# Kernel optimization log

Hardware: AMD Instinct MI355X
Metric: run time of the kernel (lower is better)

## Reference

```python
import jax, jax.numpy as jnp
import numpy as np

D = 1024
B = 16
SP = 256
T = B * SP
DT_REF = 1.0
MAX_GROWTH = 0.3


def _cayley(re, im):
    A = re + 1j * im
    A = A - A.conj().T  # skew-Hermitian part
    I = jnp.eye(A.shape[0], dtype=A.dtype)
    return jnp.linalg.solve(I + A, I - A)


def _dft_basis(d):
    n = jnp.arange(d)
    k = jnp.arange(d)[:, None]
    ang = -2.0 * jnp.pi * (k * n).astype(jnp.float32) / d
    return jnp.exp(1j * ang) / jnp.sqrt(jnp.float32(d))


def _forward(x_input, h_prev_re, h_prev_im, xg_re, xg_im, flux_re, flux_im, dt,
             u_raw_re, u_raw_im, v_raw_re, v_raw_im, log_sigma, dft_weight,
             decay_re, decay_im, Wi, bi, Wo, bo, Wg, bg,
             ld, lf, law_re, law_im, base_noise, Wu1, bu1, Wu2, bu2,
             noise_re, noise_im):
    d = x_input.shape[-1]
    # ---- basis.encode ----
    V = _cayley(v_raw_re, v_raw_im)                       # [D,D] complex
    s_diag = jnp.exp(log_sigma).astype(V.dtype)
    xc = x_input.astype(jnp.complex64)
    alpha = jax.nn.sigmoid(dft_weight)
    x_tilde = (xc @ V) * s_diag * (1.0 - alpha) + (xc @ _dft_basis(d)) * alpha
    x_tilde = x_tilde[:, None, :]                          # [T,1,D]
    # ---- flux_tracker.forward_step ----
    fdecay = jax.nn.sigmoid(decay_re) + 1j * decay_im
    x_cat = jnp.concatenate([xg_re, xg_im], axis=-1)       # [B,2D]
    xin = x_cat @ Wi.T + bi
    update = xin[..., :d] + 1j * xin[..., d:]
    flux_next = (flux_re + 1j * flux_im) * fdecay + update
    s_cat = jnp.concatenate([flux_next.real, flux_next.imag], axis=-1)
    proj = s_cat @ Wo.T + bo
    source = proj[..., :d] + 1j * proj[..., d:]            # [B,D] complex
    gate = jax.nn.sigmoid(s_cat @ Wg.T + bg)               # [B,D] real
    # ---- transition operators ----
    l_re = jnp.tanh(-jnp.exp(ld) + law_re) * MAX_GROWTH
    lam = l_re + 1j * (lf + law_im)
    dt_ratio = dt / DT_REF                                 # [1]
    op_decay = jnp.exp(lam[None, :] * dt_ratio[:, None].astype(jnp.complex64))
    op_forcing = (op_decay - 1.0) / (lam[None, :] + 1e-8)
    # ---- expand source/gate over spatial ----
    bsz = source.shape[0]
    sp = x_tilde.shape[0] // bsz
    src = jnp.broadcast_to(source[:, None, None, :], (bsz, sp, 1, d)).reshape(-1, 1, d)
    g = jnp.broadcast_to(gate[:, None, None, :], (bsz, sp, 1, d)).reshape(-1, 1, d)
    forcing = x_tilde * g + src * (1.0 - g)
    h_prev = h_prev_re + 1j * h_prev_im
    h_next = h_prev * op_decay + forcing * op_forcing      # [T,1,D]
    # ---- SDE stochastic term ----
    base_var = base_noise ** 2 * jnp.expm1(2.0 * l_re * dt_ratio[:, None]) / (2.0 * l_re + 1e-8)
    base_var = jnp.maximum(base_var, 0.0)                  # [1,D]
    h_mean = h_next.mean(axis=1).real                      # [T,D]
    u = jax.nn.softplus(jax.nn.silu(h_mean @ Wu1.T + bu1) @ Wu2.T + bu2)  # [T,D]
    std = jnp.sqrt(base_var * u)[:, None, :].astype(h_next.dtype)          # [T,1,D]
    noise = (noise_re + 1j * noise_im) * jnp.sqrt(jnp.float32(0.5))
    return h_next + noise * std, flux_next


def setup_inputs() -> dict:
    key = jax.random.key(0)
    ks = jax.random.split(key, 40)
    rn = lambda i, shp, sc=1.0: jax.random.normal(ks[i], shp, jnp.float32) * sc
    q_re = jnp.linalg.qr(rn(0, (D, D)))[0]
    q_im = jnp.linalg.qr(rn(1, (D, D)))[0]
    return {
        "x_input": rn(2, (T, D)),
        "h_prev_re": rn(3, (T, 1, D)), "h_prev_im": rn(4, (T, 1, D)),
        "xg_re": rn(5, (B, D)), "xg_im": rn(6, (B, D)),
        "flux_re": rn(7, (B, D)), "flux_im": rn(8, (B, D)),
        "dt": jnp.ones((1,), jnp.float32),
        "u_raw_re": q_re * 0.1, "u_raw_im": q_im * 0.1,
        "v_raw_re": q_re.T * 0.1, "v_raw_im": q_im.T * 0.1,
        "log_sigma": jnp.zeros((D,), jnp.float32),
        "dft_weight": jnp.float32(0.2),
        "decay_re": rn(9, (D,), 0.1) - 1.0, "decay_im": rn(10, (D,), 0.1),
        "Wi": rn(11, (2 * D, 2 * D), 0.02), "bi": jnp.zeros((2 * D,), jnp.float32),
        "Wo": rn(12, (2 * D, 2 * D), 0.02), "bo": jnp.zeros((2 * D,), jnp.float32),
        "Wg": rn(13, (D, 2 * D), 0.02), "bg": jnp.zeros((D,), jnp.float32),
        "ld": rn(14, (D,), 0.5) - 2.0, "lf": rn(15, (D,), 1.0),
        "law_re": rn(16, (D,), 0.01), "law_im": rn(17, (D,), 0.01),
        "base_noise": jnp.float32(0.01),
        "Wu1": rn(18, (D // 4, D), 0.03), "bu1": jnp.zeros((D // 4,), jnp.float32),
        "Wu2": rn(19, (D, D // 4), 0.06), "bu2": jnp.zeros((D,), jnp.float32),
        "noise_re": rn(20, (T, 1, D)), "noise_im": rn(21, (T, 1, D)),
    }


def reference(x_input, h_prev_re, h_prev_im, xg_re, xg_im, flux_re, flux_im, dt,
              u_raw_re, u_raw_im, v_raw_re, v_raw_im, log_sigma, dft_weight,
              decay_re, decay_im, Wi, bi, Wo, bo, Wg, bg,
              ld, lf, law_re, law_im, base_noise, Wu1, bu1, Wu2, bu2,
              noise_re, noise_im):
    return _forward(x_input, h_prev_re, h_prev_im, xg_re, xg_im, flux_re, flux_im, dt,
                    u_raw_re, u_raw_im, v_raw_re, v_raw_im, log_sigma, dft_weight,
                    decay_re, decay_im, Wi, bi, Wo, bo, Wg, bg,
                    ld, lf, law_re, law_im, base_noise, Wu1, bu1, Wu2, bu2,
                    noise_re, noise_im)
```

## Files before the change

kernel.cpp:

```cpp
#include <hip/hip_runtime.h>
#include <cstddef>

#define TPB 256

typedef short bf8v  __attribute__((ext_vector_type(8)));
typedef float f32x4 __attribute__((ext_vector_type(4)));
typedef unsigned short u16;

#define PSZ 2048
#define PSZ2 4096
#define LSTR 40
#define BUF1 2560
#define CSTR 68
#define RTBUF 12288

static __device__ __forceinline__ u16 f2bf(float x) {
  unsigned int u = __float_as_uint(x);
  u = (u + 0x7FFFu + ((u >> 16) & 1u)) >> 16;
  return (u16)u;
}
static __device__ __forceinline__ float bf2f(u16 x) {
  return __uint_as_float(((unsigned int)x) << 16);
}
static __device__ __forceinline__ float sigmoidf_(float x) {
  return 1.0f / (1.0f + __expf(-x));
}
static __device__ __forceinline__ float spf_(float v) {
  return (v > 15.0f) ? v : __logf(1.0f + __expf(v));
}
static __device__ __forceinline__ bf8v neg8(bf8v a) {
  #pragma unroll
  for (int i = 0; i < 8; ++i) a[i] ^= (short)0x8000;
  return a;
}
static __device__ __forceinline__ void pack8(const float4& x, const float4& y,
                                             u16* dst) {
  unsigned int* d = (unsigned int*)dst;
  d[0] = ((unsigned)f2bf(x.y) << 16) | f2bf(x.x);
  d[1] = ((unsigned)f2bf(x.w) << 16) | f2bf(x.z);
  d[2] = ((unsigned)f2bf(y.y) << 16) | f2bf(y.x);
  d[3] = ((unsigned)f2bf(y.w) << 16) | f2bf(y.z);
}
static __device__ __forceinline__ uint2 packbf4(float a, float b, float c, float d) {
  uint2 r;
  r.x = ((unsigned)f2bf(b) << 16) | f2bf(a);
  r.y = ((unsigned)f2bf(d) << 16) | f2bf(c);
  return r;
}
static __device__ __forceinline__ void gload16(const u16* g, u16* l) {
  __builtin_amdgcn_global_load_lds((const __attribute__((address_space(1))) void*)g,
                                   (__attribute__((address_space(3))) void*)l,
                                   16, 0, 0);
}
static __device__ __forceinline__ bf8v fragld(const u16* plane, int r, int kq) {
  int kb = (kq << 4) ^ (((r >> 1) & 3) << 4);
  return *(const bf8v*)(plane + r * 32 + (kb >> 1));
}
static __device__ __forceinline__ bf8v fragld2(const u16* plane, int r, int kq, int s) {
  int ch = ((s << 2) + kq) ^ (r & 7);
  return *(const bf8v*)(plane + r * 64 + (ch << 3));
}
static __device__ __forceinline__ int swz8(int flat, int T) {
  return (flat & 7) * (T >> 3) + (flat >> 3);
}

#define WAITV(n) asm volatile("s_waitcnt vmcnt(" #n ")" ::: "memory")

__global__ __launch_bounds__(TPB) void build_a_k(
    const float* __restrict__ vre, const float* __restrict__ vim,
    u16* __restrict__ Ar, u16* __restrict__ Ai,
    u16* __restrict__ Nr, u16* __restrict__ Ni)
{
  int idx = blockIdx.x * TPB + threadIdx.x;
  int i = idx >> 10, j = idx & 1023;
  float ar = vre[idx] - vre[j * 1024 + i];
  float ai = vim[idx] + vim[j * 1024 + i];
  float dg = (i == j) ? 1.0f : 0.0f;
  Ar[idx] = f2bf(ar);       Ai[idx] = f2bf(ai);
  Nr[idx] = f2bf(dg - ar);  Ni[idx] = f2bf(-ai);
}

#define CG_VARS                                                              \
  int lane = tid & 63;                                                       \
  int wr = (tid >> 7) & 1, wc = (tid >> 6) & 1;                              \
  int lr8_ = ((tid & 63) >> 3) + ((tid >> 6) << 4);                          \
  int ks2_ = (((lane & 7) ^ (lane >> 3)) << 3);                              \
  u16* Lw_ = lds + ((tid >> 6) << 10);                                       \
  f32x4 accR[2][2] = {};                                                     \
  f32x4 accI[2][2] = {};

#define CG_STAGE(buf, k0, PAr, PAi, PBr, PBi)                                \
  { u16* Lb = Lw_ + (buf) * (4 * PSZ2);                                      \
    gload16((PAr) + (size_t)(bm + lr8_) * 1024 + (k0) + ks2_,     Lb + 0 * PSZ2);       \
    gload16((PAr) + (size_t)(bm + lr8_ + 8) * 1024 + (k0) + ks2_, Lb + 0 * PSZ2 + 512); \
    gload16((PAi) + (size_t)(bm + lr8_) * 1024 + (k0) + ks2_,     Lb + 1 * PSZ2);       \
    gload16((PAi) + (size_t)(bm + lr8_ + 8) * 1024 + (k0) + ks2_, Lb + 1 * PSZ2 + 512); \
    gload16((PBr) + (size_t)(bn + lr8_) * 1024 + (k0) + ks2_,     Lb + 2 * PSZ2);       \
    gload16((PBr) + (size_t)(bn + lr8_ + 8) * 1024 + (k0) + ks2_, Lb + 2 * PSZ2 + 512); \
    gload16((PBi) + (size_t)(bn + lr8_) * 1024 + (k0) + ks2_,     Lb + 3 * PSZ2);       \
    gload16((PBi) + (size_t)(bn + lr8_ + 8) * 1024 + (k0) + ks2_, Lb + 3 * PSZ2 + 512); }

#define CG_FRAGS(buf, s)                                                     \
  const u16* L = lds + (buf) * (4 * PSZ2);                                   \
  int rA = wr * 32 + (lane & 15);                                            \
  int rB = wc * 32 + (lane & 15);                                            \
  int kq = lane >> 4;                                                        \
  bf8v ar[2], ai[2], br[2], bi[2];                                           \
  ar[0] = fragld2(L + 0 * PSZ2, rA, kq, s);  ar[1] = fragld2(L + 0 * PSZ2, rA + 16, kq, s); \
  ai[0] = fragld2(L + 1 * PSZ2, rA, kq, s);  ai[1] = fragld2(L + 1 * PSZ2, rA + 16, kq, s); \
  br[0] = fragld2(L + 2 * PSZ2, rB, kq, s);  br[1] = fragld2(L + 2 * PSZ2, rB + 16, kq, s); \
  bi[0] = fragld2(L + 3 * PSZ2, rB, kq, s);  bi[1] = fragld2(L + 3 * PSZ2, rB + 16, kq, s);

#define CG_MFMA_BNEG1                                                        \
  { bf8v nbi[2] = { neg8(bi[0]), neg8(bi[1]) };                              \
    _Pragma("unroll")                                                        \
    for (int mf = 0; mf < 2; ++mf)                                           \
      _Pragma("unroll")                                                      \
      for (int nf = 0; nf < 2; ++nf) {                                       \
        accR[mf][nf] = __builtin_amdgcn_mfma_f32_16x16x32_bf16(ar[mf], br[nf],  accR[mf][nf], 0, 0, 0); \
        accR[mf][nf] = __builtin_amdgcn_mfma_f32_16x16x32_bf16(ai[mf], bi[nf],  accR[mf][nf], 0, 0, 0); \
        accI[mf][nf] = __builtin_amdgcn_mfma_f32_16x16x32_bf16(ar[mf], nbi[nf], accI[mf][nf], 0, 0, 0); \
        accI[mf][nf] = __builtin_amdgcn_mfma_f32_16x16x32_bf16(ai[mf], br[nf],  accI[mf][nf], 0, 0, 0); \
      } }

#define CG_PIPELINE(MFMA_OP, PAr, PAi, PBr, PBi)                             \
  CG_STAGE(0, 0, PAr, PAi, PBr, PBi);                                        \
  _Pragma("unroll 1")                                                        \
  for (int t = 0; t < 16; ++t) {                                             \
    int bufc = t & 1;                                                        \
    if (t + 1 < 16) { CG_STAGE(bufc ^ 1, (t + 1) * 64, PAr, PAi, PBr, PBi);  \
                      WAITV(8); }                                            \
    else            { WAITV(0); }                                            \
    __builtin_amdgcn_sched_barrier(0);                                       \
    __builtin_amdgcn_s_barrier();                                            \
    __builtin_amdgcn_s_setprio(1);                                           \
    { CG_FRAGS(bufc, 0) MFMA_OP }                                            \
    { CG_FRAGS(bufc, 1) MFMA_OP }                                            \
    __builtin_amdgcn_s_setprio(0);                                           \
    __builtin_amdgcn_sched_barrier(0);                                       \
    __builtin_amdgcn_s_barrier();                                            \
  }

#define CGRT_VARS                                                            \
  int lane = tid & 63;                                                       \
  int wv = tid >> 6;                                                         \
  int wr = wv >> 1, wc = wv & 1;                                             \
  int ln8 = lane >> 3;                                                       \
  int ks2_ = (((lane & 7) ^ ln8) << 3);                                      \
  f32x4 accR[2] = {};                                                        \
  f32x4 accI[2] = {};

#define CGRT_STAGE(buf, k0, PAr, PAi, PBr, PBi)                              \
  { u16* Lb = lds + (buf) * RTBUF;                                           \
    _Pragma("unroll")                                                        \
    for (int j = 0; j < 6; ++j) {                                            \
      int idx = wv * 6 + j;                                                  \
      const u16* src; int row; int doff;                                     \
      if (idx < 16) {                                                        \
        int pl = idx >> 3, gr = idx & 7;                                     \
        src = pl ? (PAi) : (PAr);                                            \
        row = bm + gr * 8 + ln8;                                             \
        doff = pl * 4096 + gr * 512;                                         \
      } else {                                                               \
        int i2 = idx - 16;                                                   \
        int pl = i2 >> 2, gr = i2 & 3;                                       \
        src = pl ? (PBi) : (PBr);                                            \
        row = bn + gr * 8 + ln8;                                             \
        doff = 8192 + pl * 2048 + gr * 512;                                  \
      }                                                                      \
      gload16(src + (size_t)row * 1024 + (k0) + ks2_, Lb + doff);            \
    } }

#define CGRT_FRAGS(buf, s)                                                   \
  const u16* L = lds + (buf) * RTBUF;                                        \
  int rA = wr * 32 + (lane & 15);                                            \
  int rB = wc * 16 + (lane & 15);                                            \
  int kq = lane >> 4;                                                        \
  bf8v ar[2], ai[2], br1, bi1;                                               \
  ar[0] = fragld2(L, rA, kq, s);          ar[1] = fragld2(L, rA + 16, kq, s);          \
  ai[0] = fragld2(L + 4096, rA, kq, s);   ai[1] = fragld2(L + 4096, rA + 16, kq, s);   \
  br1 = fragld2(L + 8192, rB, kq, s);                                        \
  bi1 = fragld2(L + 10240, rB, kq, s);

#define CGRT_MFMA_BNEG0                                                      \
  { bf8v nbr = neg8(br1);                                                    \
    bf8v nbi = neg8(bi1);                                                    \
    _Pragma("unroll")                                                        \
    for (int mf = 0; mf < 2; ++mf) {                                         \
      accR[mf] = __builtin_amdgcn_mfma_f32_16x16x32_bf16(ar[mf], nbr, accR[mf], 0, 0, 0); \
      accR[mf] = __builtin_amdgcn_mfma_f32_16x16x32_bf16(ai[mf], nbi, accR[mf], 0, 0, 0); \
      accI[mf] = __builtin_amdgcn_mfma_f32_16x16x32_bf16(ar[mf], bi1, accI[mf], 0, 0, 0); \
      accI[mf] = __builtin_amdgcn_mfma_f32_16x16x32_bf16(ai[mf], nbr, accI[mf], 0, 0, 0); \
    } }

#define CGRT_MFMA_BNEG1                                                      \
  { bf8v nbi = neg8(bi1);                                                    \
    _Pragma("unroll")                                                        \
    for (int mf = 0; mf < 2; ++mf) {                                         \
      accR[mf] = __builtin_amdgcn_mfma_f32_16x16x32_bf16(ar[mf], br1, accR[mf], 0, 0, 0); \
      accR[mf] = __builtin_amdgcn_mfma_f32_16x16x32_bf16(ai[mf], bi1, accR[mf], 0, 0, 0); \
      accI[mf] = __builtin_amdgcn_mfma_f32_16x16x32_bf16(ar[mf], nbi, accI[mf], 0, 0, 0); \
      accI[mf] = __builtin_amdgcn_mfma_f32_16x16x32_bf16(ai[mf], br1, accI[mf], 0, 0, 0); \
    } }

#define CGRT_PIPELINE(MFMA_OP, PAr, PAi, PBr, PBi)                           \
  CGRT_STAGE(0, 0, PAr, PAi, PBr, PBi);                                      \
  _Pragma("unroll 1")                                                        \
  for (int t = 0; t < 16; ++t) {                                             \
    int bufc = t & 1;                                                        \
    if (t + 1 < 16) { CGRT_STAGE(bufc ^ 1, (t + 1) * 64, PAr, PAi, PBr, PBi);\
                      WAITV(6); }                                            \
    else            { WAITV(0); }                                            \
    __builtin_amdgcn_sched_barrier(0);                                       \
    __builtin_amdgcn_s_barrier();                                            \
    __builtin_amdgcn_s_setprio(1);                                           \
    { CGRT_FRAGS(bufc, 0) MFMA_OP }                                          \
    { CGRT_FRAGS(bufc, 1) MFMA_OP }                                          \
    __builtin_amdgcn_s_setprio(0);                                           \
    __builtin_amdgcn_sched_barrier(0);                                       \
    __builtin_amdgcn_s_barrier();                                            \
  }

__global__ __launch_bounds__(TPB) void d2_k(
    const u16* __restrict__ Apr, const u16* __restrict__ Api,
    u16* __restrict__ A2r, u16* __restrict__ A2i,
    const float* __restrict__ X, const float* __restrict__ Wu1,
    const float* __restrict__ Wu2,
    const float* __restrict__ ld, const float* __restrict__ lf,
    const float* __restrict__ law_re, const float* __restrict__ law_im,
    const float* __restrict__ dt, const float* __restrict__ base_noise,
    u16* __restrict__ Xb, u16* __restrict__ Wu1b, u16* __restrict__ Wu2b,
    float* __restrict__ od_re, float* __restrict__ od_im,
    float* __restrict__ of_re, float* __restrict__ of_im,
    float* __restrict__ bvar,
    const float* __restrict__ xg_re, const float* __restrict__ xg_im,
    const float* __restrict__ Wi, float* __restrict__ PpI)
{
  __shared__ __align__(16) u16 lds[2 * RTBUF];
  int tid = threadIdx.x;
  int bx = blockIdx.x;
  if (bx < 512) {
    int flat = swz8(bx, 512);
    int bm = (flat >> 5) * 64, bn = (flat & 31) * 32;
    CGRT_VARS
    CGRT_PIPELINE(CGRT_MFMA_BNEG0, Apr, Api, Apr, Api)
    #pragma unroll
    for (int mf = 0; mf < 2; ++mf) {
      int col = bn + wc * 16 + (lane & 15);
      #pragma unroll
      for (int r = 0; r < 4; ++r) {
        int rowg = bm + wr * 32 + mf * 16 + (lane >> 4) * 4 + r;
        size_t o = (size_t)rowg * 1024 + col;
        A2r[o] = f2bf(accR[mf][r]);
        A2i[o] = f2bf(accI[mf][r]);
      }
    }
  } else if (bx < 2816) {
    int e = ((bx - 512) * TPB + tid) << 3;
    const float* src;
    u16* dst;
    if (e < 4194304)       { src = X + e;               dst = Xb + e; }
    else if (e < 4456448)  { src = Wu1 + (e - 4194304); dst = Wu1b + (e - 4194304); }
    else                   { src = Wu2 + (e - 4456448); dst = Wu2b + (e - 4456448); }
    float4 a = *(const float4*)src;
    float4 b = *(const float4*)(src + 4);
    u16 tmp[8];
    pack8(a, b, tmp);
    *(bf8v*)dst = *(bf8v*)tmp;
  } else if (bx < 2820) {
    int d = (bx - 2816) * TPB + tid;
    float dtr = dt[0];
    float lre = tanhf(-expf(ld[d]) + law_re[d]) * 0.3f;
    float lim = lf[d] + law_im[d];
    float er = expf(lre * dtr);
    float sn, cs;
    sincosf(lim * dtr, &sn, &cs);
    float odr = er * cs, odi = er * sn;
    od_re[d] = odr;  od_im[d] = odi;
    float numr = odr - 1.0f, numi = odi;
    float denr = lre + 1e-8f, deni = lim;
    float inv = 1.0f / (denr * denr + deni * deni);
    of_re[d] = (numr * denr + numi * deni) * inv;
    of_im[d] = (numi * denr - numr * deni) * inv;
    float bn2 = base_noise[0];
    float bv = bn2 * bn2 * expm1f(2.0f * lre * dtr) / (2.0f * lre + 1e-8f);
    bvar[d] = fmaxf(bv, 0.0f);
  } else {
    int id = bx - 2820;
    int c0 = (id & 31) * 64;
    int kbase = (id >> 5) * 256;
    int lane = tid & 63;
    int w = tid >> 6;
    int row = tid >> 2, kq = (tid & 3) << 3;

    f32x4 acc = {};
    float4 pb0, pb1;
    u16* sl = lds;

    auto gload = [&](int k0) {
      const float* p = Wi + (size_t)(c0 + row) * 2048 + k0 + kq;
      pb0 = *(const float4*)p; pb1 = *(const float4*)(p + 4);
    };
    auto stolds = [&](int buf) {
      pack8(pb0, pb1, sl + buf * BUF1 + row * LSTR + kq);
    };
    auto compute = [&](int buf, int k0) {
      int ar = lane & 15;
      int ko = (lane >> 4) * 8;
      const float* ap = (k0 < 1024) ? (xg_re + (size_t)ar * 1024 + k0 + ko)
                                    : (xg_im + (size_t)ar * 1024 + k0 + ko - 1024);
      float4 a0 = *(const float4*)ap, a1 = *(const float4*)(ap + 4);
      u16 abuf[8];
      pack8(a0, a1, abuf);
      bf8v af = *(bf8v*)abuf;
      bf8v bfr = *(const bf8v*)(sl + buf * BUF1 + (w * 16 + (lane & 15)) * LSTR + ko);
      acc = __builtin_amdgcn_mfma_f32_16x16x32_bf16(af, bfr, acc, 0, 0, 0);
    };

    gload(kbase); stolds(0); __syncthreads();
    int cur = 0;
    for (int t = 0; t < 8; ++t) {
      int k0 = kbase + t * 32;
      if (t < 7) gload(k0 + 32);
      compute(cur, k0);
      if (t < 7) stolds(cur ^ 1);
      __syncthreads();
      cur ^= 1;
    }
    int c = c0 + w * 16 + (lane & 15);
    #pragma unroll
    for (int r = 0; r < 4; ++r) {
      int rr = (lane >> 4) * 4 + r;
      PpI[((size_t)(id >> 5) * 16 + rr) * 2048 + c] = acc[r];
    }
  }
}

__global__ __launch_bounds__(TPB) void d3_k(
    const u16* __restrict__ A2r, const u16* __restrict__ A2i,
    const u16* __restrict__ Nr2, const u16* __restrict__ Ni2,
    u16* __restrict__ A4r, u16* __restrict__ A4i,
    u16* __restrict__ T1r, u16* __restrict__ T1i,
    const float* __restrict__ PpI, const float* __restrict__ bi,
    const float* __restrict__ flux_re, const float* __restrict__ flux_im,
    const float* __restrict__ decay_re, const float* __restrict__ decay_im,
    float* __restrict__ FNr, float* __restrict__ FNi,
    float* __restrict__ out1)
{
  __shared__ __align__(16) u16 lds[2 * 4 * PSZ2];
  int tid = threadIdx.x;
  int bx = blockIdx.x;
  if (bx < 512) {
    int flat = swz8(bx, 512);
    int z = flat >> 8;
    int t8 = flat & 255;
    int bm = (t8 >> 4) * 64, bn = (t8 & 15) * 64;
    const u16* Apr = z ? Nr2 : A2r;
    const u16* Api = z ? Ni2 : A2i;
    u16* Cr16 = z ? T1r : A4r;
    u16* Ci16 = z ? T1i : A4i;
    CG_VARS
    CG_PIPELINE(CG_MFMA_BNEG1, Apr, Api, A2r, A2i)
    #pragma unroll
    for (int mf = 0; mf < 2; ++mf)
      #pragma unroll
      for (int nf = 0; nf < 2; ++nf) {
        int col = bn + wc * 32 + nf * 16 + (lane & 15);
        #pragma unroll
        for (int r = 0; r < 4; ++r) {
          int rowg = bm + wr * 32 + mf * 16 + (lane >> 4) * 4 + r;
          size_t o = (size_t)rowg * 1024 + col;
          float vr = accR[mf][nf][r], vi = accI[mf][nf][r];
          if (z) { vr += bf2f(Nr2[o]); vi += bf2f(Ni2[o]); }
          Cr16[o] = f2bf(vr);
          Ci16[o] = f2bf(vi);
        }
      }
  } else {
    int idx = (bx - 512) * TPB + tid;
    int b = idx >> 10, d = idx & 1023;
    float ur = bi[d];
    float ui = bi[1024 + d];
    #pragma unroll
    for (int s = 0; s < 8; ++s) {
      ur += PpI[(size_t)s * 32768 + b * 2048 + d];
      ui += PpI[(size_t)s * 32768 + b * 2048 + 1024 + d];
    }
    float fdr = sigmoidf_(decay_re[d]);
    float fdi = decay_im[d];
    float fr = flux_re[idx], fi = flux_im[idx];
    float nr = fr * fdr - fi * fdi + ur;
    float ni = fr * fdi + fi * fdr + ui;
    FNr[idx] = nr;  FNi[idx] = ni;
    out1[idx] = nr;
  }
}

__global__ __launch_bounds__(TPB) void d4_k(
    const u16* __restrict__ T1r, const u16* __restrict__ T1i,
    const u16* __restrict__ A4r, const u16* __restrict__ A4i,
    const float* __restrict__ log_sigma, const float* __restrict__ dft_weight,
    u16* __restrict__ Mtr, u16* __restrict__ Mti,
    const float* __restrict__ FNr, const float* __restrict__ FNi,
    const float* __restrict__ Wo, const float* __restrict__ Wg,
    float* __restrict__ PpO, float* __restrict__ PpG)
{
  __shared__ __align__(16) u16 lds[2 * RTBUF];
  int tid = threadIdx.x;
  int bx = blockIdx.x;
  if (bx < 512) {
    int flat = swz8(bx, 512);
    int bm = (flat >> 5) * 64, bn = (flat & 31) * 32;
    CGRT_VARS
    CGRT_PIPELINE(CGRT_MFMA_BNEG1, T1r, T1i, A4r, A4i)

    u16* mtLr = lds;
    u16* mtLi = lds + 2304;
    __syncthreads();
    {
      float alpha = sigmoidf_(dft_weight[0]);
      const float isq = 0.03125f * alpha;
      #pragma unroll
      for (int mf = 0; mf < 2; ++mf) {
        int dl = wc * 16 + (lane & 15);
        int dgl = bn + dl;
        float w1 = expf(log_sigma[dgl]) * (1.0f - alpha);
        #pragma unroll
        for (int r = 0; r < 4; ++r) {
          int kl = wr * 32 + mf * 16 + (lane >> 4) * 4 + r;
          int kgl = bm + kl;
          size_t o = (size_t)kgl * 1024 + dgl;
          float dg = (kgl == dgl) ? 1.0f : 0.0f;
          float vr = 2.0f * accR[mf][r] + 2.0f * bf2f(T1r[o]) - dg;
          float vi = 2.0f * accI[mf][r] + 2.0f * bf2f(T1i[o]);
          int mm = (kgl * dgl) & 1023;
          float ang = -6.283185307179586f * (float)mm * (1.0f / 1024.0f);
          float sn, cs;
          sincosf(ang, &sn, &cs);
          mtLr[dl * 72 + kl] = f2bf(vr * w1 + cs * isq);
          mtLi[dl * 72 + kl] = f2bf(vi * w1 + sn * isq);
        }
      }
    }
    __syncthreads();
    {
      int dl = tid >> 3, kl0 = (tid & 7) * 8;
      size_t o = (size_t)(bn + dl) * 1024 + bm + kl0;
      *(uint4*)(Mtr + o) = *(uint4*)(mtLr + dl * 72 + kl0);
      *(uint4*)(Mti + o) = *(uint4*)(mtLi + dl * 72 + kl0);
    }
  } else {
    int id = bx - 512;
    int cb = id % 48;
    int ky = id / 48;
    const float* Bw = (cb < 32) ? Wo : Wg;
    float* Pp = (cb < 32) ? PpO : PpG;
    int N = (cb < 32) ? 2048 : 1024;
    int c0 = ((cb < 32) ? cb : (cb - 32)) * 64;
    int kbase = ky * 256;
    int lane = tid & 63;
    int w = tid >> 6;
    int row = tid >> 2, kq = (tid & 3) << 3;

    f32x4 acc = {};
    float4 pb0, pb1;
    u16* sl = lds;

    auto gload = [&](int k0) {
      const float* p = Bw + (size_t)(c0 + row) * 2048 + k0 + kq;
      pb0 = *(const float4*)p; pb1 = *(const float4*)(p + 4);
    };
    auto stolds = [&](int buf) {
      pack8(pb0, pb1, sl + buf * BUF1 + row * LSTR + kq);
    };
    auto compute = [&](int buf, int k0) {
      int ar = lane & 15;
      int ko = (lane >> 4) * 8;
      const float* ap = (k0 < 1024) ? (FNr + (size_t)ar * 1024 + k0 + ko)
                                    : (FNi + (size_t)ar * 1024 + k0 + ko - 1024);
      float4 a0 = *(const float4*)ap, a1 = *(const float4*)(ap + 4);
      u16 abuf[8];
      pack8(a0, a1, abuf);
      bf8v af = *(bf8v*)abuf;
      bf8v bfr = *(const bf8v*)(sl + buf * BUF1 + (w * 16 + (lane & 15)) * LSTR + ko);
      acc = __builtin_amdgcn_mfma_f32_16x16x32_bf16(af, bfr, acc, 0, 0, 0);
    };

    gload(kbase); stolds(0); __syncthreads();
    int cur = 0;
    for (int t = 0; t < 8; ++t) {
      int k0 = kbase + t * 32;
      if (t < 7) gload(k0 + 32);
      compute(cur, k0);
      if (t < 7) stolds(cur ^ 1);
      __syncthreads();
      cur ^= 1;
    }
    int c = c0 + w * 16 + (lane & 15);
    #pragma unroll
    for (int r = 0; r < 4; ++r) {
      int rr = (lane >> 4) * 4 + r;
      Pp[((size_t)ky * 16 + rr) * N + c] = acc[r];
    }
  }
}

__global__ __launch_bounds__(TPB) void xmh_nt_k(
    const u16* __restrict__ Xb,
    const u16* __restrict__ Mtr, const u16* __restrict__ Mti,
    const float* __restrict__ PpO, const float* __restrict__ PpG,
    const float* __restrict__ bo, const float* __restrict__ bg,
    const float* __restrict__ od_re, const float* __restrict__ od_im,
    const float* __restrict__ of_re, const float* __restrict__ of_im,
    const float* __restrict__ hp_re, const float* __restrict__ hp_im,
    u16* __restrict__ Hrb)
{
  __shared__ __align__(16) u16 lds[2 * 16384];
  int flat = swz8(blockIdx.x, 512);
  int bm = (flat >> 4) * 128, bn = (flat & 15) * 64;
  int tid = threadIdx.x;
  int lane = tid & 63;
  int w = tid >> 6;
  int wr = w >> 1, wc = w & 1;
  int ln8 = lane >> 3;
  int ks2_ = (((lane & 7) ^ ln8) << 3);

  f32x4 accR[4][2] = {};
  f32x4 accI[4][2] = {};

#define XM_STAGE(buf, k0)                                                    \
  { u16* Lb = lds + (buf) * 16384;                                           \
    _Pragma("unroll")                                                        \
    for (int g = 0; g < 4; ++g)                                              \
      gload16(Xb + (size_t)(bm + w * 32 + g * 8 + ln8) * 1024 + (k0) + ks2_, \
              Lb + (w * 32 + g * 8) * 64);                                   \
    _Pragma("unroll")                                                        \
    for (int g = 0; g < 2; ++g) {                                            \
      gload16(Mtr + (size_t)(bn + w * 16 + g * 8 + ln8) * 1024 + (k0) + ks2_,\
              Lb + 8192 + (w * 16 + g * 8) * 64);                            \
      gload16(Mti + (size_t)(bn + w * 16 + g * 8 + ln8) * 1024 + (k0) + ks2_,\
              Lb + 12288 + (w * 16 + g * 8) * 64);                           \
    } }
#define XM_COMPUTE(buf, s)                                                   \
  { const u16* L = lds + (buf) * 16384;                                      \
    int kq = lane >> 4;                                                      \
    bf8v a[4], br[2], bi[2];                                                 \
    _Pragma("unroll")                                                        \
    for (int mf = 0; mf < 4; ++mf)                                           \
      a[mf] = fragld2(L, wr * 64 + mf * 16 + (lane & 15), kq, s);            \
    _Pragma("unroll")                                                        \
    for (int nf = 0; nf < 2; ++nf) {                                         \
      br[nf] = fragld2(L + 8192,  wc * 32 + nf * 16 + (lane & 15), kq, s);   \
      bi[nf] = fragld2(L + 12288, wc * 32 + nf * 16 + (lane & 15), kq, s);   \
    }                                                                        \
    _Pragma("unroll")                                                        \
    for (int mf = 0; mf < 4; ++mf)                                           \
      _Pragma("unroll")                                                      \
      for (int nf = 0; nf < 2; ++nf) {                                       \
        accR[mf][nf] = __builtin_amdgcn_mfma_f32_16x16x32_bf16(a[mf], br[nf], accR[mf][nf], 0, 0, 0); \
        accI[mf][nf] = __builtin_amdgcn_mfma_f32_16x16x32_bf16(a[mf], bi[nf], accI[mf][nf], 0, 0, 0); \
      } }

  XM_STAGE(0, 0);
  #pragma unroll 1
  for (int t = 0; t < 16; ++t) {
    int bufc = t & 1;
    if (t + 1 < 16) { XM_STAGE(bufc ^ 1, (t + 1) * 64); WAITV(8); }
    else            { WAITV(0); }
    __builtin_amdgcn_sched_barrier(0);
    __builtin_amdgcn_s_barrier();
    __builtin_amdgcn_s_setprio(1);
    XM_COMPUTE(bufc, 0)
    XM_COMPUTE(bufc, 1)
    __builtin_amdgcn_s_setprio(0);
    __builtin_amdgcn_sched_barrier(0);
    __builtin_amdgcn_s_barrier();
  }

  float* gl  = (float*)lds;
  float* prl = gl + 64;
  float* pil = prl + 64;
  __syncthreads();
  if (tid < 64) {
    int c = bn + tid;
    int b0 = bm >> 8;
    float vg = bg[c];
    float vr = bo[c];
    float vi = bo[1024 + c];
    #pragma unroll
    for (int s = 0; s < 8; ++s) {
      vg += PpG[(size_t)s * 16384 + b0 * 1024 + c];
      vr += PpO[(size_t)s * 32768 + b0 * 2048 + c];
      vi += PpO[(size_t)s * 32768 + b0 * 2048 + 1024 + c];
    }
    gl[tid]  = sigmoidf_(vg);
    prl[tid] = vr;
    pil[tid] = vi;
  }
  __syncthreads();

  #pragma unroll
  for (int mf = 0; mf < 4; ++mf)
    #pragma unroll
    for (int nf = 0; nf < 2; ++nf) {
      int lc = wc * 32 + nf * 16 + (lane & 15);
      int c = bn + lc;
      float g  = gl[lc];
      float sr = prl[lc];
      float si = pil[lc];
      float odr = od_re[c], odi = od_im[c];
      float ofr = of_re[c], ofi = of_im[c];
      #pragma unroll
      for (int r = 0; r < 4; ++r) {
        int t = bm + wr * 64 + mf * 16 + (lane >> 4) * 4 + r;
        float fr = accR[mf][nf][r] * g + sr * (1.0f - g);
        float fi = accI[mf][nf][r] * g + si * (1.0f - g);
        size_t off = (size_t)t * 1024 + c;
        float pr = hp_re[off], pi = hp_im[off];
        Hrb[off] = f2bf(pr * odr - pi * odi + fr * ofr - fi * ofi);
      }
    }
}

template<int KI, int EPI>
__global__ __launch_bounds__(TPB) void rgemm_nt_k(
    const u16* __restrict__ A, const u16* __restrict__ B,
    const float* __restrict__ bias,
    u16* __restrict__ C16, int nbxl, int total,
    const u16* __restrict__ HrbF, const float* __restrict__ nre,
    const float* __restrict__ bvarp, float* __restrict__ outp)
{
  __shared__ __align__(16) u16 lds[3 * 2 * PSZ];
  const int K = KI * 32;
  int tid = threadIdx.x;
  int flat = swz8(blockIdx.x, total);
  int bm = (flat >> nbxl) * 64;
  int bn = (flat & ((1 << nbxl) - 1)) * 64;
  const int N = 64 << nbxl;
  int lane = tid & 63;
  int wr = (tid >> 7) & 1, wc = (tid >> 6) & 1;
  int lr_ = ((tid & 63) >> 2) + ((tid >> 6) << 4);
  int ks_ = (((tid & 3) ^ ((tid >> 3) & 3)) << 3);
  u16* Lw_ = lds + ((tid >> 6) << 9);

  f32x4 acc[2][2] = {};

#define RG_STAGE(buf, k0)                                                    \
  { u16* Lb = Lw_ + (buf) * (2 * PSZ);                                       \
    gload16(A + (size_t)(bm + lr_) * K + (k0) + ks_, Lb + 0 * PSZ);          \
    gload16(B + (size_t)(bn + lr_) * K + (k0) + ks_, Lb + 1 * PSZ); }
#define RG_COMPUTE(buf)                                                      \
  { const u16* L = lds + (buf) * (2 * PSZ);                                  \
    int rA = wr * 32 + (lane & 15);                                          \
    int rB = wc * 32 + (lane & 15);                                          \
    int kq = lane >> 4;                                                      \
    bf8v a[2], b[2];                                                         \
    a[0] = fragld(L + 0 * PSZ, rA, kq);  a[1] = fragld(L + 0 * PSZ, rA + 16, kq); \
    b[0] = fragld(L + 1 * PSZ, rB, kq);  b[1] = fragld(L + 1 * PSZ, rB + 16, kq); \
    _Pragma("unroll")                                                        \
    for (int mf = 0; mf < 2; ++mf)                                           \
      _Pragma("unroll")                                                      \
      for (int nf = 0; nf < 2; ++nf)                                         \
        acc[mf][nf] = __builtin_amdgcn_mfma_f32_16x16x32_bf16(a[mf], b[nf], acc[mf][nf], 0, 0, 0); }

  RG_STAGE(0, 0);
  RG_STAGE(1, 32);
  #pragma unroll 1
  for (int t = 0; t < KI; ++t) {
    int bufc = t % 3;
    if (t + 2 < KI) { RG_STAGE((t + 2) % 3, (t + 2) * 32); }
    if (t + 2 < KI)      { WAITV(4); }
    else if (t + 1 < KI) { WAITV(2); }
    else                 { WAITV(0); }
    __builtin_amdgcn_sched_barrier(0);
    __builtin_amdgcn_s_barrier();
    __builtin_amdgcn_s_setprio(1);
    RG_COMPUTE(bufc)
    __builtin_amdgcn_s_setprio(0);
    __builtin_amdgcn_sched_barrier(0);
    __builtin_amdgcn_s_barrier();
  }

  if constexpr (EPI == 0) {
    #pragma unroll
    for (int mf = 0; mf < 2; ++mf)
      #pragma unroll
      for (int nf = 0; nf < 2; ++nf) {
        int c = bn + wc * 32 + nf * 16 + (lane & 15);
        #pragma unroll
        for (int r = 0; r < 4; ++r) {
          int t = bm + wr * 32 + mf * 16 + (lane >> 4) * 4 + r;
          float v = acc[mf][nf][r] + bias[c];
          v = v * sigmoidf_(v);
          C16[(size_t)t * N + c] = f2bf(v);
        }
      }
  } else {
    float* ct = (float*)lds;
    __syncthreads();
    #pragma unroll
    for (int mf = 0; mf < 2; ++mf)
      #pragma unroll
      for (int nf = 0; nf < 2; ++nf) {
        int rbase = wr * 32 + mf * 16 + (lane >> 4) * 4;
        int cc = wc * 32 + nf * 16 + (lane & 15);
        #pragma unroll
        for (int r = 0; r < 4; ++r)
          ct[(rbase + r) * CSTR + cc] = acc[mf][nf][r];
      }
    __syncthreads();
    int w = tid >> 6, l = tid & 63;
    int lcol = (l & 15) * 4;
    const float s2 = 0.7071067811865476f;
    #pragma unroll
    for (int p = 0; p < 4; ++p) {
      int lrow = w * 16 + p * 4 + (l >> 4);
      int t = bm + lrow;
      int c = bn + lcol;
      float4 v4 = *(float4*)&ct[lrow * CSTR + lcol];
      float4 bi4 = *(const float4*)(bias + c);
      float u0 = spf_(v4.x + bi4.x);
      float u1 = spf_(v4.y + bi4.y);
      float u2 = spf_(v4.z + bi4.z);
      float u3 = spf_(v4.w + bi4.w);
      size_t off = (size_t)t * 1024 + c;
      uint2 hb2 = *(const uint2*)(HrbF + off);
      float4 nr4 = *(const float4*)(nre + off);
      float4 bv4 = *(const float4*)(bvarp + c);
      float4 o;
      o.x = bf2f((u16)(hb2.x & 0xFFFF)) + nr4.x * sqrtf(bv4.x * u0) * s2;
      o.y = bf2f((u16)(hb2.x >> 16))    + nr4.y * sqrtf(bv4.y * u1) * s2;
      o.z = bf2f((u16)(hb2.y & 0xFFFF)) + nr4.z * sqrtf(bv4.z * u2) * s2;
      o.w = bf2f((u16)(hb2.y >> 16))    + nr4.w * sqrtf(bv4.w * u3) * s2;
      *(float4*)(outp + off) = o;
    }
  }
}

extern "C" void kernel_launch(void* const* d_in, const int* in_sizes, int n_in,
                              void* d_out, int out_size, void* d_ws, size_t ws_size,
                              hipStream_t stream) {
  (void)in_sizes; (void)n_in; (void)out_size;

  const float* x_input    = (const float*)d_in[0];
  const float* h_prev_re  = (const float*)d_in[1];
  const float* h_prev_im  = (const float*)d_in[2];
  const float* xg_re      = (const float*)d_in[3];
  const float* xg_im      = (const float*)d_in[4];
  const float* flux_re    = (const float*)d_in[5];
  const float* flux_im    = (const float*)d_in[6];
  const float* dt         = (const float*)d_in[7];
  const float* v_raw_re   = (const float*)d_in[10];
  const float* v_raw_im   = (const float*)d_in[11];
  const float* log_sigma  = (const float*)d_in[12];
  const float* dft_weight = (const float*)d_in[13];
  const float* decay_re   = (const float*)d_in[14];
  const float* decay_im   = (const float*)d_in[15];
  const float* Wi_in      = (const float*)d_in[16];
  const float* bi         = (const float*)d_in[17];
  const float* Wo         = (const float*)d_in[18];
  const float* bo         = (const float*)d_in[19];
  const float* Wg         = (const float*)d_in[20];
  const float* bg         = (const float*)d_in[21];
  const float* ld         = (const float*)d_in[22];
  const float* lf         = (const float*)d_in[23];
  const float* law_re     = (const float*)d_in[24];
  const float* law_im     = (const float*)d_in[25];
  const float* base_noise = (const float*)d_in[26];
  const float* Wu1        = (const float*)d_in[27];
  const float* bu1        = (const float*)d_in[28];
  const float* Wu2        = (const float*)d_in[29];
  const float* bu2        = (const float*)d_in[30];
  const float* noise_re   = (const float*)d_in[31];

  const size_t PL16 = 1024ull * 1024ull;
  if (ws_size < 16 * PL16 * 2) return;

  u16* P = (u16*)d_ws;
  u16* Ar  = P + 0 * PL16;   u16* Ai  = P + 1 * PL16;
  u16* Nr  = P + 2 * PL16;   u16* Ni  = P + 3 * PL16;
  u16* A2r = P + 4 * PL16;   u16* A2i = P + 5 * PL16;
  u16* A4r = P + 6 * PL16;   u16* A4i = P + 7 * PL16;
  u16* T1r = P + 8 * PL16;   u16* T1i = P + 9 * PL16;
  u16* Mtr = P + 2 * PL16;   u16* Mti = P + 3 * PL16;
  u16* Xb  = P + 10 * PL16;
  u16* Hrb = P + 4 * PL16;
  float* PpO = (float*)(P + 0 * PL16);
  float* PpG = PpO + 262144;
  float* PpI = (float*)(P + 14 * PL16);
  u16* mlp1b = P + 14 * PL16;
  u16* Wu1b  = P + 15 * PL16;
  u16* Wu2b  = Wu1b + 262144;
  float* sm  = (float*)(P + 15 * PL16 + 524288);
  float* FNr  = sm;
  float* FNi  = FNr + 16384;
  float* od_re = FNi + 16384;
  float* od_im = od_re + 1024;
  float* of_re = od_im + 1024;
  float* of_im = of_re + 1024;
  float* bvar  = of_im + 1024;

  float* out0f = (float*)d_out;
  float* out1f = out0f + (size_t)4096 * 1024;

  build_a_k<<<4096, TPB, 0, stream>>>(v_raw_re, v_raw_im, Ar, Ai, Nr, Ni);
  d2_k<<<3076, TPB, 0, stream>>>(Ar, Ai, A2r, A2i,
                                 x_input, Wu1, Wu2,
                                 ld, lf, law_re, law_im, dt, base_noise,
                                 Xb, Wu1b, Wu2b,
                                 od_re, od_im, of_re, of_im, bvar,
                                 xg_re, xg_im, Wi_in, PpI);
  d3_k<<<576, TPB, 0, stream>>>(A2r, A2i, Nr, Ni, A4r, A4i, T1r, T1i,
                                PpI, bi, flux_re, flux_im, decay_re, decay_im,
                                FNr, FNi, out1f);
  d4_k<<<896, TPB, 0, stream>>>(T1r, T1i, A4r, A4i, log_sigma, dft_weight,
                                Mtr, Mti,
                                FNr, FNi, Wo, Wg, PpO, PpG);
  xmh_nt_k<<<512, TPB, 0, stream>>>(Xb, Mtr, Mti, PpO, PpG, bo, bg,
                                    od_re, od_im, of_re, of_im,
                                    h_prev_re, h_prev_im, Hrb);
  rgemm_nt_k<32, 0><<<256, TPB, 0, stream>>>(Hrb, Wu1b, bu1, mlp1b, 2, 256,
                                             nullptr, nullptr, nullptr, nullptr);
  rgemm_nt_k<8, 2><<<1024, TPB, 0, stream>>>(mlp1b, Wu2b, bu2, nullptr, 4, 1024,
                                             Hrb, noise_re, bvar, out0f);
}
```

Before: 119.6 us.

## Switch xmh_nt_k to triple-buffered K=32 LDS pipeline with prefetch depth two

The K-loop in xmh_nt_k now moves 32-wide K slices through three LDS buffers instead of 64-wide slices through two, keeping two stages of global loads in flight while the current buffer feeds the MFMAs. The load mapping is rebuilt so each wave issues four 16-byte loads across X, Mtr and Mti, and it uses a new XOR swizzle matched to the single-fragment loader. This aims to hide global memory latency better and cut LDS use (48KB down to 48KB-equivalent smaller tiles, allowing more occupancy). In exchange the kernel runs twice as many barriers per K, and the vmcnt bookkeeping becomes more delicate.

```diff
diff --git a/kernel.cpp b/kernel.cpp
--- a/kernel.cpp
+++ b/kernel.cpp
@@ -13,6 +13,7 @@
 #define BUF1 2560
 #define CSTR 68
 #define RTBUF 12288
+#define XBUF 8192
 
 static __device__ __forceinline__ u16 f2bf(float x) {
   unsigned int u = __float_as_uint(x);
@@ -515,43 +516,44 @@
     const float* __restrict__ hp_re, const float* __restrict__ hp_im,
     u16* __restrict__ Hrb)
 {
-  __shared__ __align__(16) u16 lds[2 * 16384];
+  __shared__ __align__(16) u16 lds[3 * XBUF];
   int flat = swz8(blockIdx.x, 512);
   int bm = (flat >> 4) * 128, bn = (flat & 15) * 64;
   int tid = threadIdx.x;
   int lane = tid & 63;
-  int w = tid >> 6;
-  int wr = w >> 1, wc = w & 1;
-  int ln8 = lane >> 3;
-  int ks2_ = (((lane & 7) ^ ln8) << 3);
+  int wv = tid >> 6;
+  int wr = wv >> 1, wc = wv & 1;
+  int lr4 = lane >> 2;
+  int ks_ = (((lane & 3) ^ ((lane >> 3) & 3)) << 3);
 
   f32x4 accR[4][2] = {};
   f32x4 accI[4][2] = {};
 
 #define XM_STAGE(buf, k0)                                                    \
-  { u16* Lb = lds + (buf) * 16384;                                           \
+  { u16* Lb = lds + (buf) * XBUF;                                            \
     _Pragma("unroll")                                                        \
-    for (int g = 0; g < 4; ++g)                                              \
-      gload16(Xb + (size_t)(bm + w * 32 + g * 8 + ln8) * 1024 + (k0) + ks2_, \
-              Lb + (w * 32 + g * 8) * 64);                                   \
-    _Pragma("unroll")                                                        \
-    for (int g = 0; g < 2; ++g) {                                            \
-      gload16(Mtr + (size_t)(bn + w * 16 + g * 8 + ln8) * 1024 + (k0) + ks2_,\
-              Lb + 8192 + (w * 16 + g * 8) * 64);                            \
-      gload16(Mti + (size_t)(bn + w * 16 + g * 8 + ln8) * 1024 + (k0) + ks2_,\
-              Lb + 12288 + (w * 16 + g * 8) * 64);                           \
+    for (int j = 0; j < 4; ++j) {                                            \
+      int idx = wv * 4 + j;                                                  \
+      const u16* src; int row; int doff;                                     \
+      if (idx < 8)       { src = Xb;  row = bm + idx * 16 + lr4;                    \
+                           doff = idx * 512; }                               \
+      else if (idx < 12) { src = Mtr; row = bn + (idx - 8) * 16 + lr4;              \
+                           doff = 4096 + (idx - 8) * 512; }                  \
+      else               { src = Mti; row = bn + (idx - 12) * 16 + lr4;             \
+                           doff = 6144 + (idx - 12) * 512; }                 \
+      gload16(src + (size_t)row * 1024 + (k0) + ks_, Lb + doff);             \
     } }
-#define XM_COMPUTE(buf, s)                                                   \
-  { const u16* L = lds + (buf) * 16384;                                      \
+#define XM_COMPUTE(buf)                                                      \
+  { const u16* L = lds + (buf) * XBUF;                                       \
     int kq = lane >> 4;                                                      \
     bf8v a[4], br[2], bi[2];                                                 \
     _Pragma("unroll")                                                        \
     for (int mf = 0; mf < 4; ++mf)                                           \
-      a[mf] = fragld2(L, wr * 64 + mf * 16 + (lane & 15), kq, s);            \
+      a[mf] = fragld(L, wr * 64 + mf * 16 + (lane & 15), kq);                \
     _Pragma("unroll")                                                        \
     for (int nf = 0; nf < 2; ++nf) {                                         \
-      br[nf] = fragld2(L + 8192,  wc * 32 + nf * 16 + (lane & 15), kq, s);   \
-      bi[nf] = fragld2(L + 12288, wc * 32 + nf * 16 + (lane & 15), kq, s);   \
+      br[nf] = fragld(L + 4096, wc * 32 + nf * 16 + (lane & 15), kq);        \
+      bi[nf] = fragld(L + 6144, wc * 32 + nf * 16 + (lane & 15), kq);        \
     }                                                                        \
     _Pragma("unroll")                                                        \
     for (int mf = 0; mf < 4; ++mf)                                           \
@@ -562,16 +564,18 @@
       } }
 
   XM_STAGE(0, 0);
+  XM_STAGE(1, 32);
   #pragma unroll 1
-  for (int t = 0; t < 16; ++t) {
-    int bufc = t & 1;
-    if (t + 1 < 16) { XM_STAGE(bufc ^ 1, (t + 1) * 64); WAITV(8); }
-    else            { WAITV(0); }
+  for (int t = 0; t < 32; ++t) {
+    int bufc = t % 3;
+    if (t + 2 < 32) { XM_STAGE((t + 2) % 3, (t + 2) * 32); }
+    if (t + 2 < 32)      { WAITV(8); }
+    else if (t + 1 < 32) { WAITV(4); }
+    else                 { WAITV(0); }
     __builtin_amdgcn_sched_barrier(0);
     __builtin_amdgcn_s_barrier();
     __builtin_amdgcn_s_setprio(1);
-    XM_COMPUTE(bufc, 0)
-    XM_COMPUTE(bufc, 1)
+    XM_COMPUTE(bufc)
     __builtin_amdgcn_s_setprio(0);
     __builtin_amdgcn_sched_barrier(0);
     __builtin_amdgcn_s_barrier();
```

New measurement: 122.8 us. +2.7%, slower.
